# Optimization experiments

Hardware: AMD Instinct MI355X
Metric: run time of the kernel (lower is better)

## Reference

```python
import jax, jax.numpy as jnp
import numpy as np

D = 512      # latent channels (d)
K = 512      # codebook size (k)
PATCH = 8    # encoder conv kernel/stride


def _nearest_embed(z, W):
    """z: (B, D, H, W) latents; W: (D, K) codebook. Returns (quantized (B,D,H,W), argmin (B,H,W))."""
    B, d, H, Wd = z.shape
    zf = z.transpose(0, 2, 3, 1).reshape(-1, d)                      # (N, D)
    # squared L2 distances to each code: ||z||^2 - 2 z.W + ||e||^2
    d2 = (jnp.sum(zf * zf, axis=1, keepdims=True)
          - 2.0 * (zf @ W)
          + jnp.sum(W * W, axis=0))                                   # (N, K)
    idx = jnp.argmin(d2, axis=1)                                      # (N,)
    q = jnp.take(W.T, idx, axis=0)                                    # gather: (N, D)
    q = q.reshape(B, H, Wd, d).transpose(0, 3, 1, 2)
    return q, idx.reshape(B, H, Wd)


def _encode(x, enc_w, enc_b):
    z = jax.lax.conv_general_dilated(x, enc_w, window_strides=(PATCH, PATCH),
                                     padding='VALID',
                                     dimension_numbers=('NCHW', 'OIHW', 'NCHW'))
    return z + enc_b[None, :, None, None]


def _decode(z, dec_w, dec_b):
    y = jax.lax.conv_transpose(z, dec_w, strides=(PATCH, PATCH), padding='VALID',
                               dimension_numbers=('NCHW', 'IOHW', 'NCHW'))
    return y + dec_b[None, :, None, None]


def setup_inputs() -> dict:
    key = jax.random.key(0)
    k1, k2, k3, k4 = jax.random.split(key, 4)
    x = jax.random.normal(k1, (32, 3, 256, 256), dtype=jnp.float32)
    enc_w = jax.random.normal(k2, (D, 3, PATCH, PATCH), dtype=jnp.float32) * 0.02
    enc_b = jnp.zeros((D,), jnp.float32)
    dec_w = jax.random.normal(k3, (D, 3, PATCH, PATCH), dtype=jnp.float32) * 0.02  # IOHW
    dec_b = jnp.zeros((3,), jnp.float32)
    # embedding.weight.normal_(0, 0.02); torch.fmod(weight, 0.04)
    emb_w = jnp.fmod(jax.random.normal(k4, (D, K), dtype=jnp.float32) * 0.02, 0.04)
    return {"x": x, "enc_w": enc_w, "enc_b": enc_b,
            "dec_w": dec_w, "dec_b": dec_b, "emb_w": emb_w}


def reference(x, enc_w, enc_b, dec_w, dec_b, emb_w):
    z_e = _encode(x, enc_w, enc_b)                                    # (32, 512, 32, 32)
    # lookup 1: weight_sg=True (codebook grad stopped) + straight-through estimator
    q1, argmin = _nearest_embed(z_e, jax.lax.stop_gradient(emb_w))
    z_q = z_e + jax.lax.stop_gradient(q1 - z_e)
    # lookup 2: detached encoder output, grads flow to codebook via scatter-add
    emb, _ = _nearest_embed(jax.lax.stop_gradient(z_e), emb_w)
    recon = _decode(z_q, dec_w, dec_b)                                # (32, 3, 256, 256)
    return recon, z_e, emb, argmin
```

## Files before the change

### kernel.cpp

```cpp
#include <hip/hip_runtime.h>
#include <cfloat>

#define PIXB 1024
static const size_t OFF_Z = 6291456;
static const size_t OFF_E = 23068672;
static const size_t OFF_A = 39845888;

typedef __attribute__((address_space(1))) const unsigned int cg_u32;
typedef __attribute__((address_space(3))) unsigned int l_u32;
typedef _Float16 f16x8 __attribute__((ext_vector_type(8)));
typedef _Float16 f16x4 __attribute__((ext_vector_type(4)));
typedef float f32x16 __attribute__((ext_vector_type(16)));

#define SPLIT_SCALE 4096.0f
#define SPLIT_INV   (1.0f / 4096.0f)

#define GL16(srcp, dstp) __builtin_amdgcn_global_load_lds((cg_u32*)(srcp), (l_u32*)(dstp), 16, 0, 0)

__global__ __launch_bounds__(256) void k_prep(const float* __restrict__ W,
                                              const float* __restrict__ dw,
                                              const float* __restrict__ ew,
                                              _Float16* __restrict__ wq,
                                              float* __restrict__ w2,
                                              _Float16* __restrict__ aq,
                                              _Float16* __restrict__ wrow,
                                              _Float16* __restrict__ dwh,
                                              int do_aux) {
  const int t = threadIdx.x;
  const int bx = blockIdx.x;
  __shared__ float T[64][65];
  __shared__ float T2[128][65];
  if (bx < 32) {
    __shared__ float TS[32][260];
    const int cp = bx >> 4, ch = bx & 15;
#pragma unroll
    for (int i = 0; i < 32; ++i)
      TS[i][t] = W[(size_t)(ch * 32 + i) * 512 + cp * 256 + t];
    __syncthreads();
#pragma unroll
    for (int j = 0; j < 4; ++j) {
      const int u = j * 256 + t;
      const int c = u >> 2, slot = u & 3;
      const int se = slot ^ ((c >> 1) & 3);
      f16x8 h, l;
#pragma unroll
      for (int jj = 0; jj < 8; ++jj) {
        const float v = TS[slot * 8 + jj][c];
        const _Float16 hh = (_Float16)v;
        h[jj] = hh;
        l[jj] = (_Float16)((v - (float)hh) * SPLIT_SCALE);
      }
      _Float16* base = wq + cp * 262144 + ch * 16384 + c * 32 + se * 8;
      *(f16x8*)(base) = h;
      *(f16x8*)(base + 8192) = l;
    }
    return;
  }
  if (bx < 34) {
    const int k = (bx - 32) * 256 + t;
    float acc = 0.f;
    for (int d = 0; d < 512; ++d) { const float v = W[(size_t)d * 512 + k]; acc = fmaf(v, v, acc); }
    w2[k] = acc;
    return;
  }
  if (bx < 46) {
    const int ch = bx - 34;
#pragma unroll
    for (int cc = 0; cc < 2; ++cc) {
      const int c = cc * 256 + t;
      const float* src = ew + (size_t)c * 192 + ch * 16;
#pragma unroll
      for (int slot = 0; slot < 2; ++slot) {
        f16x8 h, l;
#pragma unroll
        for (int j = 0; j < 8; ++j) {
          const float v = src[slot * 8 + j];
          const _Float16 hh = (_Float16)v;
          h[j] = hh;
          l[j] = (_Float16)((v - (float)hh) * SPLIT_SCALE);
        }
        const int se = slot ^ ((c >> 2) & 1);
        _Float16* dst = aq + (size_t)ch * 16384 + c * 16 + se * 8;
        *(f16x8*)dst = h;
        *(f16x8*)(dst + 8192) = l;
      }
    }
    return;
  }
  if (!do_aux) return;
  if (bx < 110) {
    const int id = bx - 46;
    const int c0 = (id & 7) * 64, d0 = (id >> 3) * 64;
#pragma unroll
    for (int i = 0; i < 16; ++i) {
      const int dl = i * 4 + (t >> 6);
      T[dl][t & 63] = W[(size_t)(d0 + dl) * 512 + c0 + (t & 63)];
    }
    __syncthreads();
#pragma unroll
    for (int i = 0; i < 16; ++i) {
      const int cl = i * 4 + (t >> 6);
      const int dl = t & 63;
      wrow[(size_t)(c0 + cl) * 512 + d0 + dl] = (_Float16)T[dl][cl];
    }
    return;
  }
  {
    const int id = bx - 110;
    const int m0 = (id % 3) * 64, d0 = (id / 3) * 128;
#pragma unroll
    for (int i = 0; i < 32; ++i) {
      const int idx = i * 256 + t;
      const int dl = idx >> 6, ml = idx & 63;
      T2[dl][ml] = dw[(size_t)(d0 + dl) * 192 + m0 + ml];
    }
    __syncthreads();
#pragma unroll
    for (int i = 0; i < 32; ++i) {
      const int idx = i * 256 + t;
      const int ml = idx >> 7, dl = idx & 127;
      dwh[(size_t)(m0 + ml) * 512 + d0 + dl] = (_Float16)T2[dl][ml];
    }
  }
}

__global__ __launch_bounds__(512) void k_encmfma(const float* __restrict__ x,
                                                 const _Float16* __restrict__ aq,
                                                 const float* __restrict__ eb,
                                                 _Float16* __restrict__ zq2,
                                                 float* __restrict__ out) {
  __shared__ __align__(16) unsigned char CB[131072];
  __shared__ float ebL[512];
  const int t = threadIdx.x;
  ebL[t] = eb[t];
  const int w = t >> 6, lane = t & 63;
  const int wc = w & 3, wp = w >> 2;
  const int n0 = blockIdx.x * 64;
  const int b = n0 >> 10, pixbase = n0 & 1023;
  const int i0 = pixbase >> 5;
  const int row = lane & 31, hi = lane >> 5;

  int ab[4];
#pragma unroll
  for (int ct = 0; ct < 4; ++ct) {
    const int c = wc * 128 + ct * 32 + row;
    ab[ct] = c * 32 + ((hi ^ ((c >> 2) & 1)) << 4);
  }
  const int u = t & 255, srow = u >> 6, vsl = u & 63;
  const int csrc = vsl ^ ((vsl >> 3) & 1);
  const float* xb = x + ((size_t)b * 3 * 256 + (i0 + (srow >> 1)) * 8 + (srow & 1)) * 256 + csrc * 4;
  const int bv0 = (((2 * row) ^ ((row >> 2) & 1)) << 4);
  const int bv1 = (((2 * row + 1) ^ ((row >> 2) & 1)) << 4);
  const int brb = wp * 4096 + (wp * 2 + hi) * 1024;

  f32x16 accA[4], accB[4];
#pragma unroll
  for (int ct = 0; ct < 4; ++ct) { accA[ct] = (f32x16)(0.0f); accB[ct] = (f32x16)(0.0f); }

#define STAGE_A(chv) { const _Float16* as_ = aq + (size_t)(chv) * 16384 + t * 8;            \
    char* ad_ = (char*)CB + ((chv) % 3) * 32768 + t * 16;                                   \
    GL16(as_, ad_); GL16(as_ + 4096, ad_ + 8192);                                           \
    GL16(as_ + 8192, ad_ + 16384); GL16(as_ + 12288, ad_ + 24576); }
#define STAGE_B(chv) GL16(xb + (((chv) >> 2) * 65536 + ((chv) & 3) * 512),                  \
                          (char*)CB + 98304 + (((chv) & 3)) * 8192 + t * 16)
#define ECOMP(chv)                                                                          \
  { const char* abuf = (const char*)CB + ((chv) % 3) * 32768;                               \
    const char* bbuf = (const char*)CB + 98304 + ((chv) & 3) * 8192 + brb;                  \
    const float4 xa = *(const float4*)(bbuf + bv0);                                         \
    const float4 xc = *(const float4*)(bbuf + bv1);                                         \
    const float xs[8] = {xa.x, xa.y, xa.z, xa.w, xc.x, xc.y, xc.z, xc.w};                   \
    f16x8 Bh, Bl;                                                                           \
    _Pragma("unroll") for (int q = 0; q < 8; ++q) {                                         \
      const _Float16 hh = (_Float16)xs[q];                                                  \
      Bh[q] = hh; Bl[q] = (_Float16)((xs[q] - (float)hh) * SPLIT_SCALE); }                  \
    __builtin_amdgcn_s_setprio(1);                                                          \
    _Pragma("unroll") for (int ct_ = 0; ct_ < 4; ++ct_) {                                   \
      const f16x8 Ah = *(const f16x8*)(abuf + ab[ct_]);                                     \
      const f16x8 Al = *(const f16x8*)(abuf + 16384 + ab[ct_]);                             \
      accA[ct_] = __builtin_amdgcn_mfma_f32_32x32x16_f16(Ah, Bh, accA[ct_], 0, 0, 0);       \
      accB[ct_] = __builtin_amdgcn_mfma_f32_32x32x16_f16(Ah, Bl, accB[ct_], 0, 0, 0);       \
      accB[ct_] = __builtin_amdgcn_mfma_f32_32x32x16_f16(Al, Bh, accB[ct_], 0, 0, 0); }     \
    __builtin_amdgcn_s_setprio(0); }
#define EPHASE(chv, waitlit)                                                                \
  { asm volatile("s_waitcnt vmcnt(" #waitlit ")" ::: "memory");                             \
    __builtin_amdgcn_sched_barrier(0);                                                      \
    __builtin_amdgcn_s_barrier();                                                           \
    ECOMP(chv);                                                                             \
    __builtin_amdgcn_s_barrier(); }

  STAGE_A(0); STAGE_B(0);
  STAGE_A(1); STAGE_B(1);
  STAGE_B(2);
#pragma unroll 1
  for (int ch = 0; ch < 9; ++ch) {
    STAGE_A(ch + 2);
    STAGE_B(ch + 3);
    EPHASE(ch, 11);
  }
  STAGE_A(11);
  EPHASE(9, 10);
  EPHASE(10, 5);
  EPHASE(11, 0);
#undef STAGE_A
#undef STAGE_B
#undef ECOMP
#undef EPHASE

  __syncthreads();
  _Float16* ZB = (_Float16*)CB;
  const int pl = wp * 32 + row;
#pragma unroll
  for (int ct = 0; ct < 4; ++ct) {
    float zv[16];
#pragma unroll
    for (int r = 0; r < 16; ++r) {
      const int c = wc * 128 + ct * 32 + (r & 3) + ((r >> 2) << 3) + (hi << 2);
      zv[r] = fmaf(accB[ct][r], SPLIT_INV, accA[ct][r]) + ebL[c];
      out[OFF_Z + ((size_t)(b * 512 + c)) * 1024 + pixbase + pl] = zv[r];
    }
#pragma unroll
    for (int rq = 0; rq < 4; ++rq) {
      f16x4 vh, vl;
#pragma unroll
      for (int q = 0; q < 4; ++q) {
        const float f = zv[rq * 4 + q];
        const _Float16 hh = (_Float16)f;
        vh[q] = hh;
        vl[q] = (_Float16)((f - (float)hh) * SPLIT_SCALE);
      }
      const int c4 = wc * 128 + ct * 32 + (rq << 3) + (hi << 2);
      const int off = pl * 1024 + ((c4 * 2) ^ ((pl & 7) << 4));
      *(f16x4*)((char*)ZB + off) = vh;
      *(f16x4*)((char*)ZB + 65536 + off) = vl;
    }
  }
  __syncthreads();
#pragma unroll
  for (int spl = 0; spl < 2; ++spl)
#pragma unroll
    for (int gg = 0; gg < 8; ++gg) {
      const int g = w * 8 + gg;
      const f16x8 vv = *(const f16x8*)((char*)ZB + spl * 65536 + lane * 1024 + ((g * 16) ^ ((lane & 7) << 4)));
      *(f16x8*)(zq2 + ((size_t)(spl * 64 + g) * 32768 + b * 1024 + pixbase + lane) * 8) = vv;
    }
}

__global__ __launch_bounds__(512) void k_dist(const _Float16* __restrict__ wq,
                                              const _Float16* __restrict__ zq,
                                              const float* __restrict__ w2ws,
                                              float* __restrict__ out) {
  __shared__ __align__(16) unsigned char CB[131072];
  __shared__ float WV[512];
  __shared__ int   WI[512];
  const int t = threadIdx.x;
  const int w = t >> 6, lane = t & 63;
  const int wc = w & 3, wp = w >> 2;
  const int n0 = blockIdx.x * 64;
  const int b = n0 >> 10, pixbase = n0 & 1023;
  const int row = lane & 31, hi = lane >> 5;
  const int kl16 = hi << 4;
  const int pl = wp * 32 + row;

  int abase[2][2];
#pragma unroll
  for (int ct = 0; ct < 2; ++ct) {
    const int cl = wc * 64 + ct * 32 + row;
    const int sw = ((cl >> 1) & 3) << 4;
#pragma unroll
    for (int ks = 0; ks < 2; ++ks)
      abase[ct][ks] = cl * 64 + (((ks << 5) | kl16) ^ sw);
  }
  const _Float16* zsrc0 = zq + ((size_t)((t >> 8) * 64 + ((t >> 6) & 3)) * 32768 +
                                b * 1024 + pixbase + (t & 63)) * 8;

#define STAGE_W(cpv, chv)                                                        \
  { const _Float16* ws_ = wq + (cpv) * 262144 + (chv) * 16384 + t * 8;           \
    char* wd_ = (char*)CB + ((chv) % 3) * 32768 + t * 16;                        \
    GL16(ws_, wd_); GL16(ws_ + 4096, wd_ + 8192);                                \
    GL16(ws_ + 8192, wd_ + 16384); GL16(ws_ + 12288, wd_ + 24576); }
#define STAGE_Z(chv)                                                             \
  GL16(zsrc0 + (size_t)(chv) * 1048576,                                          \
       (char*)CB + 98304 + ((chv) & 3) * 8192 + t * 16)
#define COMPUTE(chv)                                                             \
  { const char* wb_ = (const char*)CB + ((chv) % 3) * 32768;                     \
    const char* zb_ = (const char*)CB + 98304 + ((chv) & 3) * 8192;              \
    const f16x8 Bh0 = *(const f16x8*)(zb_ + hi * 1024 + pl * 16);                \
    const f16x8 Bh1 = *(const f16x8*)(zb_ + (2 + hi) * 1024 + pl * 16);          \
    const f16x8 Bl0 = *(const f16x8*)(zb_ + 4096 + hi * 1024 + pl * 16);         \
    const f16x8 Bl1 = *(const f16x8*)(zb_ + 4096 + (2 + hi) * 1024 + pl * 16);   \
    __builtin_amdgcn_s_setprio(1);                                               \
    _Pragma("unroll")                                                            \
    for (int ct_ = 0; ct_ < 2; ++ct_) {                                          \
      const f16x8 Ah0 = *(const f16x8*)(wb_ + abase[ct_][0]);                    \
      const f16x8 Al0 = *(const f16x8*)(wb_ + 16384 + abase[ct_][0]);            \
      const f16x8 Ah1 = *(const f16x8*)(wb_ + abase[ct_][1]);                    \
      const f16x8 Al1 = *(const f16x8*)(wb_ + 16384 + abase[ct_][1]);            \
      accA[ct_] = __builtin_amdgcn_mfma_f32_32x32x16_f16(Ah0, Bh0, accA[ct_], 0, 0, 0); \
      accB[ct_] = __builtin_amdgcn_mfma_f32_32x32x16_f16(Ah0, Bl0, accB[ct_], 0, 0, 0); \
      accB[ct_] = __builtin_amdgcn_mfma_f32_32x32x16_f16(Al0, Bh0, accB[ct_], 0, 0, 0); \
      accA[ct_] = __builtin_amdgcn_mfma_f32_32x32x16_f16(Ah1, Bh1, accA[ct_], 0, 0, 0); \
      accB[ct_] = __builtin_amdgcn_mfma_f32_32x32x16_f16(Ah1, Bl1, accB[ct_], 0, 0, 0); \
      accB[ct_] = __builtin_amdgcn_mfma_f32_32x32x16_f16(Al1, Bh1, accB[ct_], 0, 0, 0); \
    }                                                                            \
    __builtin_amdgcn_s_setprio(0); }
#define PHASE(chv, waitlit)                                                      \
  { asm volatile("s_waitcnt vmcnt(" #waitlit ")" ::: "memory");                  \
    __builtin_amdgcn_sched_barrier(0);                                           \
    __builtin_amdgcn_s_barrier();                                                \
    COMPUTE(chv);                                                                \
    __builtin_amdgcn_s_barrier(); }

  float bv = FLT_MAX; int bi = 0x7fffffff;

#pragma unroll 1
  for (int cp = 0; cp < 2; ++cp) {
    f32x16 accA[2], accB[2];
#pragma unroll
    for (int ct = 0; ct < 2; ++ct) { accA[ct] = (f32x16)(0.0f); accB[ct] = (f32x16)(0.0f); }
    STAGE_W(cp, 0); STAGE_Z(0);
    STAGE_W(cp, 1); STAGE_Z(1);
    STAGE_Z(2);
#pragma unroll 1
    for (int ch = 0; ch < 13; ++ch) {
      STAGE_W(cp, ch + 2);
      STAGE_Z(ch + 3);
      PHASE(ch, 11);
    }
    STAGE_W(cp, 15);
    PHASE(13, 10);
    PHASE(14, 5);
    PHASE(15, 0);

#pragma unroll
    for (int ct = 0; ct < 2; ++ct) {
#pragma unroll
      for (int r = 0; r < 16; ++r) {
        const int code = cp * 256 + wc * 64 + ct * 32 +
                         ((r & 3) + ((r >> 2) << 3) + (hi << 2));
        const float zw = fmaf(accB[ct][r], SPLIT_INV, accA[ct][r]);
        const float d2 = fmaf(-2.f, zw, w2ws[code]);
        if (d2 < bv || (d2 == bv && code < bi)) { bv = d2; bi = code; }
      }
    }
  }
#undef STAGE_W
#undef STAGE_Z
#undef COMPUTE
#undef PHASE

  WV[w * 64 + lane] = bv;
  WI[w * 64 + lane] = bi;
  __syncthreads();
  if (t < 64) {
    const int pw = t >> 5;
    float fbv = FLT_MAX; int fbi = 0x7fffffff;
#pragma unroll
    for (int wcc = 0; wcc < 4; ++wcc)
#pragma unroll
      for (int hh = 0; hh < 2; ++hh) {
        const int li = (pw * 4 + wcc) * 64 + (t & 31) + hh * 32;
        const float v = WV[li];
        const int ii = WI[li];
        if (v < fbv || (v == fbv && ii < fbi)) { fbv = v; fbi = ii; }
      }
    out[OFF_A + n0 + t] = (float)fbi;
  }
}

__global__ __launch_bounds__(256) void k_gather(const float* __restrict__ Wc,
                                                float* __restrict__ out) {
  const int n0 = blockIdx.x * 32;
  const int b = n0 >> 10, pixbase = n0 & 1023;
  const int t = threadIdx.x;
  const int pix = t & 31;
  const int kidx = (int)out[OFF_A + n0 + pix];
  for (int d = t >> 5; d < 512; d += 8)
    out[OFF_E + ((size_t)(b * 512 + d)) * 1024 + pixbase + pix] = Wc[(size_t)d * 512 + kidx];
}

__global__ __launch_bounds__(512) void k_decmfma(const _Float16* __restrict__ wrow,
                                                 const _Float16* __restrict__ dwh,
                                                 const float* __restrict__ db,
                                                 float* __restrict__ out) {
  __shared__ __align__(16) _Float16 QB[2][4096];
  __shared__ int KIDX[128];
  const int t = threadIdx.x;
  const int w = t >> 6, lane = t & 63;
  const int pt = w & 3, mg = w >> 2;
  const int blk = blockIdx.x;
  const int b = blk >> 3;
  const int pixbase = (blk & 7) * 128;
  if (t < 128) KIDX[t] = (int)out[OFF_A + b * 1024 + pixbase + t];
  __syncthreads();
  const int pixS = t >> 2, slotS = t & 3;
  const _Float16* qsrc = wrow + (size_t)KIDX[pixS] * 512 + slotS * 8;
  const int ldsW = pixS * 32 + (slotS ^ ((pixS >> 1) & 3)) * 8;

  const _Float16* abp[3];
#pragma unroll
  for (int mt = 0; mt < 3; ++mt)
    abp[mt] = dwh + (size_t)((mg * 3 + mt) * 32 + (lane & 31)) * 512 + ((lane >> 5) << 3);

  const int brow = pt * 32 + (lane & 31);
  const int bsw = (brow >> 1) & 3;
  int boff[2];
#pragma unroll
  for (int ks = 0; ks < 2; ++ks)
    boff[ks] = brow * 32 + (((ks * 2 + (lane >> 5)) ^ bsw)) * 8;

  f32x16 acc[3];
#pragma unroll
  for (int mt = 0; mt < 3; ++mt) acc[mt] = (f32x16)(0.0f);
  f16x8 A[2][3][2];
  f16x8 qd[2];

  qd[0] = *(const f16x8*)(qsrc);
#pragma unroll
  for (int mt = 0; mt < 3; ++mt)
#pragma unroll
    for (int ks = 0; ks < 2; ++ks)
      A[0][mt][ks] = *(const f16x8*)(abp[mt] + ks * 16);
  *(f16x8*)&QB[0][ldsW] = qd[0];
  qd[1] = *(const f16x8*)(qsrc + 32);
  __syncthreads();

#pragma unroll
  for (int ch = 0; ch < 16; ++ch) {
    const int par = ch & 1;
    if (ch < 15) {
      *(f16x8*)&QB[par ^ 1][ldsW] = qd[(ch + 1) & 1];
#pragma unroll
      for (int mt = 0; mt < 3; ++mt)
#pragma unroll
        for (int ks = 0; ks < 2; ++ks)
          A[par ^ 1][mt][ks] = *(const f16x8*)(abp[mt] + (ch + 1) * 32 + ks * 16);
    }
    if (ch < 14) qd[ch & 1] = *(const f16x8*)(qsrc + (ch + 2) * 32);
    const f16x8 B0 = *(const f16x8*)&QB[par][boff[0]];
    const f16x8 B1 = *(const f16x8*)&QB[par][boff[1]];
#pragma unroll
    for (int mt = 0; mt < 3; ++mt) {
      acc[mt] = __builtin_amdgcn_mfma_f32_32x32x16_f16(A[par][mt][0], B0, acc[mt], 0, 0, 0);
      acc[mt] = __builtin_amdgcn_mfma_f32_32x32x16_f16(A[par][mt][1], B1, acc[mt], 0, 0, 0);
    }
    __syncthreads();
  }

  const float b0 = db[0], b1 = db[1], b2 = db[2];
  const int pix = pixbase + pt * 32 + (lane & 31);
  const int i = pix >> 5, j = pix & 31;
#pragma unroll
  for (int mt = 0; mt < 3; ++mt) {
    const int m0 = (mg * 3 + mt) * 32;
#pragma unroll
    for (int r = 0; r < 16; ++r) {
      const int m = m0 + (r & 3) + ((r >> 2) << 3) + ((lane >> 5) << 2);
      const int c = m >> 6, ki = (m >> 3) & 7, kj = m & 7;
      const float bias = (c == 0) ? b0 : ((c == 1) ? b1 : b2);
      out[(((size_t)b * 3 + c) * 256 + i * 8 + 7 - ki) * 256 + j * 8 + 7 - kj] = acc[mt][r] + bias;
    }
  }
}

__global__ __launch_bounds__(256) void k_decode(const float* __restrict__ dw,
                                                const float* __restrict__ db,
                                                float* out) {
  __shared__ __align__(16) float Qs[32][132];
  __shared__ __align__(16) float Ws3[32][68];
  const int n0 = blockIdx.x * 128;
  const int b = n0 / PIXB, pixbase = n0 % PIXB;
  const int mt = blockIdx.y;
  const int t = threadIdx.x;
  const int pg = t & 31, ck = t >> 5;
  float acc[4][8];
#pragma unroll
  for (int p = 0; p < 4; ++p)
#pragma unroll
    for (int k = 0; k < 8; ++k) acc[p][k] = 0.f;
  for (int dc = 0; dc < 16; ++dc) {
#pragma unroll
    for (int ii = 0; ii < 4; ++ii) {
      const int id = t + ii * 256;
      const int dd = id >> 5, p4 = id & 31;
      *reinterpret_cast<float4*>(&Qs[dd][p4 * 4]) =
        *reinterpret_cast<const float4*>(&out[OFF_E + ((size_t)b * 512 + dc * 32 + dd) * 1024 + pixbase + p4 * 4]);
    }
#pragma unroll
    for (int ii = 0; ii < 2; ++ii) {
      const int id = t + ii * 256;
      const int dd = id >> 4, m4 = id & 15;
      *reinterpret_cast<float4*>(&Ws3[dd][m4 * 4]) =
        *reinterpret_cast<const float4*>(&dw[(size_t)(dc * 32 + dd) * 192 + mt * 64 + m4 * 4]);
    }
    __syncthreads();
#pragma unroll
    for (int dd = 0; dd < 32; ++dd) {
      const float4 qv = *reinterpret_cast<const float4*>(&Qs[dd][pg * 4]);
      const float4 wa = *reinterpret_cast<const float4*>(&Ws3[dd][ck * 8]);
      const float4 wb = *reinterpret_cast<const float4*>(&Ws3[dd][ck * 8 + 4]);
      const float q[4] = {qv.x, qv.y, qv.z, qv.w};
      const float wv[8] = {wa.x, wa.y, wa.z, wa.w, wb.x, wb.y, wb.z, wb.w};
#pragma unroll
      for (int p = 0; p < 4; ++p)
#pragma unroll
        for (int k = 0; k < 8; ++k) acc[p][k] = fmaf(q[p], wv[k], acc[p][k]);
    }
    __syncthreads();
  }
  const int ckg = mt * 8 + ck;
  const int c = ckg >> 3, ki = ckg & 7;
  const float bias = db[c];
#pragma unroll
  for (int p = 0; p < 4; ++p) {
    const int pix = pixbase + pg * 4 + p;
    const int i = pix >> 5, j = pix & 31;
    const size_t base = (((size_t)b * 3 + c) * 256 + i * 8 + 7 - ki) * 256 + j * 8;
#pragma unroll
    for (int kj = 0; kj < 8; ++kj) out[base + 7 - kj] = acc[p][kj] + bias;
  }
}

extern "C" void kernel_launch(void* const* d_in, const int* in_sizes, int n_in,
                              void* d_out, int out_size, void* d_ws, size_t ws_size,
                              hipStream_t stream) {
  const float* x     = (const float*)d_in[0];
  const float* enc_w = (const float*)d_in[1];
  const float* enc_b = (const float*)d_in[2];
  const float* dec_w = (const float*)d_in[3];
  const float* dec_b = (const float*)d_in[4];
  const float* emb_w = (const float*)d_in[5];
  float* out = (float*)d_out;
  float* w2 = (float*)d_ws;
  _Float16* wrow = (_Float16*)((char*)d_ws + 2048);
  _Float16* dwh  = (_Float16*)((char*)d_ws + 2048 + 524288);
  const int do_aux = (ws_size >= (size_t)(2048 + 524288 + 196608)) ? 1 : 0;
  _Float16* wq  = (_Float16*)d_out;
  _Float16* aq  = (_Float16*)((char*)d_out + 2097152);
  _Float16* zq2 = (_Float16*)((char*)d_out + 92274688);

  k_prep<<<122, 256, 0, stream>>>(emb_w, dec_w, enc_w, wq, w2, aq, wrow, dwh, do_aux);
  k_encmfma<<<512, 512, 0, stream>>>(x, aq, enc_b, zq2, out);
  k_dist<<<512, 512, 0, stream>>>(wq, zq2, w2, out);
  k_gather<<<1024, 256, 0, stream>>>(emb_w, out);
  if (do_aux)
    k_decmfma<<<256, 512, 0, stream>>>(wrow, dwh, dec_b, out);
  else
    k_decode<<<dim3(256, 3), 256, 0, stream>>>(dec_w, dec_b, out);
}
```

Before: 208.4 us.

## Read fp32 z_e directly in distance kernel and fuse codebook gather

The encoder no longer writes a separate split-fp16 (hi/lo) copy of z_e to scratch. The distance kernel now stages the fp32 z_e output tile into LDS and does the hi/lo fp16 split on the fly before the MFMAs. The separate gather kernel is folded into the tail of the distance kernel, which keeps argmin indices in shared memory. This removes a scratch write and read pass plus one launch, in exchange for extra conversion ALU work inside the MFMA loop and a possibly bank-conflicted LDS access pattern for the fp32 reads.

```diff
diff --git a/kernel.cpp b/kernel.cpp
--- a/kernel.cpp
+++ b/kernel.cpp
@@ -9,7 +9,6 @@
 typedef __attribute__((address_space(1))) const unsigned int cg_u32;
 typedef __attribute__((address_space(3))) unsigned int l_u32;
 typedef _Float16 f16x8 __attribute__((ext_vector_type(8)));
-typedef _Float16 f16x4 __attribute__((ext_vector_type(4)));
 typedef float f32x16 __attribute__((ext_vector_type(16)));
 
 #define SPLIT_SCALE 4096.0f
@@ -127,7 +126,6 @@
 __global__ __launch_bounds__(512) void k_encmfma(const float* __restrict__ x,
                                                  const _Float16* __restrict__ aq,
                                                  const float* __restrict__ eb,
-                                                 _Float16* __restrict__ zq2,
                                                  float* __restrict__ out) {
   __shared__ __align__(16) unsigned char CB[131072];
   __shared__ float ebL[512];
@@ -206,59 +204,32 @@
 #undef ECOMP
 #undef EPHASE
 
-  __syncthreads();
-  _Float16* ZB = (_Float16*)CB;
   const int pl = wp * 32 + row;
 #pragma unroll
   for (int ct = 0; ct < 4; ++ct) {
-    float zv[16];
 #pragma unroll
     for (int r = 0; r < 16; ++r) {
       const int c = wc * 128 + ct * 32 + (r & 3) + ((r >> 2) << 3) + (hi << 2);
-      zv[r] = fmaf(accB[ct][r], SPLIT_INV, accA[ct][r]) + ebL[c];
-      out[OFF_Z + ((size_t)(b * 512 + c)) * 1024 + pixbase + pl] = zv[r];
-    }
-#pragma unroll
-    for (int rq = 0; rq < 4; ++rq) {
-      f16x4 vh, vl;
-#pragma unroll
-      for (int q = 0; q < 4; ++q) {
-        const float f = zv[rq * 4 + q];
-        const _Float16 hh = (_Float16)f;
-        vh[q] = hh;
-        vl[q] = (_Float16)((f - (float)hh) * SPLIT_SCALE);
-      }
-      const int c4 = wc * 128 + ct * 32 + (rq << 3) + (hi << 2);
-      const int off = pl * 1024 + ((c4 * 2) ^ ((pl & 7) << 4));
-      *(f16x4*)((char*)ZB + off) = vh;
-      *(f16x4*)((char*)ZB + 65536 + off) = vl;
-    }
-  }
-  __syncthreads();
-#pragma unroll
-  for (int spl = 0; spl < 2; ++spl)
-#pragma unroll
-    for (int gg = 0; gg < 8; ++gg) {
-      const int g = w * 8 + gg;
-      const f16x8 vv = *(const f16x8*)((char*)ZB + spl * 65536 + lane * 1024 + ((g * 16) ^ ((lane & 7) << 4)));
-      *(f16x8*)(zq2 + ((size_t)(spl * 64 + g) * 32768 + b * 1024 + pixbase + lane) * 8) = vv;
-    }
+      out[OFF_Z + ((size_t)(b * 512 + c)) * 1024 + pixbase + pl] =
+          fmaf(accB[ct][r], SPLIT_INV, accA[ct][r]) + ebL[c];
+    }
+  }
 }
 
 __global__ __launch_bounds__(512) void k_dist(const _Float16* __restrict__ wq,
-                                              const _Float16* __restrict__ zq,
+                                              const float* __restrict__ Wc,
                                               const float* __restrict__ w2ws,
                                               float* __restrict__ out) {
   __shared__ __align__(16) unsigned char CB[131072];
   __shared__ float WV[512];
   __shared__ int   WI[512];
+  __shared__ int   IDX[64];
   const int t = threadIdx.x;
   const int w = t >> 6, lane = t & 63;
   const int wc = w & 3, wp = w >> 2;
   const int n0 = blockIdx.x * 64;
   const int b = n0 >> 10, pixbase = n0 & 1023;
   const int row = lane & 31, hi = lane >> 5;
-  const int kl16 = hi << 4;
   const int pl = wp * 32 + row;
 
   int abase[2][2];
@@ -268,10 +239,9 @@
     const int sw = ((cl >> 1) & 3) << 4;
 #pragma unroll
     for (int ks = 0; ks < 2; ++ks)
-      abase[ct][ks] = cl * 64 + (((ks << 5) | kl16) ^ sw);
-  }
-  const _Float16* zsrc0 = zq + ((size_t)((t >> 8) * 64 + ((t >> 6) & 3)) * 32768 +
-                                b * 1024 + pixbase + (t & 63)) * 8;
+      abase[ct][ks] = cl * 64 + (((ks << 5) | (hi << 4)) ^ sw);
+  }
+  const float* zsrc = out + OFF_Z + ((size_t)(b * 512 + (t >> 4))) * 1024 + pixbase + (t & 15) * 4;
 
 #define STAGE_W(cpv, chv)                                                        \
   { const _Float16* ws_ = wq + (cpv) * 262144 + (chv) * 16384 + t * 8;           \
@@ -279,15 +249,19 @@
     GL16(ws_, wd_); GL16(ws_ + 4096, wd_ + 8192);                                \
     GL16(ws_ + 8192, wd_ + 16384); GL16(ws_ + 12288, wd_ + 24576); }
 #define STAGE_Z(chv)                                                             \
-  GL16(zsrc0 + (size_t)(chv) * 1048576,                                          \
+  GL16(zsrc + (size_t)(chv) * 32768,                                             \
        (char*)CB + 98304 + ((chv) & 3) * 8192 + t * 16)
 #define COMPUTE(chv)                                                             \
   { const char* wb_ = (const char*)CB + ((chv) % 3) * 32768;                     \
     const char* zb_ = (const char*)CB + 98304 + ((chv) & 3) * 8192;              \
-    const f16x8 Bh0 = *(const f16x8*)(zb_ + hi * 1024 + pl * 16);                \
-    const f16x8 Bh1 = *(const f16x8*)(zb_ + (2 + hi) * 1024 + pl * 16);          \
-    const f16x8 Bl0 = *(const f16x8*)(zb_ + 4096 + hi * 1024 + pl * 16);         \
-    const f16x8 Bl1 = *(const f16x8*)(zb_ + 4096 + (2 + hi) * 1024 + pl * 16);   \
+    f16x8 Bh0, Bl0, Bh1, Bl1;                                                    \
+    _Pragma("unroll") for (int q = 0; q < 8; ++q) {                              \
+      const float f0 = *(const float*)(zb_ + (hi * 8 + q) * 256 + pl * 4);       \
+      const _Float16 h0 = (_Float16)f0;                                          \
+      Bh0[q] = h0; Bl0[q] = (_Float16)((f0 - (float)h0) * SPLIT_SCALE);          \
+      const float f1 = *(const float*)(zb_ + (16 + hi * 8 + q) * 256 + pl * 4);  \
+      const _Float16 h1 = (_Float16)f1;                                          \
+      Bh1[q] = h1; Bl1[q] = (_Float16)((f1 - (float)h1) * SPLIT_SCALE); }        \
     __builtin_amdgcn_s_setprio(1);                                               \
     _Pragma("unroll")                                                            \
     for (int ct_ = 0; ct_ < 2; ++ct_) {                                          \
@@ -364,17 +338,13 @@
         if (v < fbv || (v == fbv && ii < fbi)) { fbv = v; fbi = ii; }
       }
     out[OFF_A + n0 + t] = (float)fbi;
-  }
-}
-
-__global__ __launch_bounds__(256) void k_gather(const float* __restrict__ Wc,
-                                                float* __restrict__ out) {
-  const int n0 = blockIdx.x * 32;
-  const int b = n0 >> 10, pixbase = n0 & 1023;
-  const int t = threadIdx.x;
-  const int pix = t & 31;
-  const int kidx = (int)out[OFF_A + n0 + pix];
-  for (int d = t >> 5; d < 512; d += 8)
+    IDX[t] = fbi;
+  }
+  __syncthreads();
+
+  const int pix = t & 63;
+  const int kidx = IDX[pix];
+  for (int d = t >> 6; d < 512; d += 8)
     out[OFF_E + ((size_t)(b * 512 + d)) * 1024 + pixbase + pix] = Wc[(size_t)d * 512 + kidx];
 }
 
@@ -536,12 +506,10 @@
   const int do_aux = (ws_size >= (size_t)(2048 + 524288 + 196608)) ? 1 : 0;
   _Float16* wq  = (_Float16*)d_out;
   _Float16* aq  = (_Float16*)((char*)d_out + 2097152);
-  _Float16* zq2 = (_Float16*)((char*)d_out + 92274688);
 
   k_prep<<<122, 256, 0, stream>>>(emb_w, dec_w, enc_w, wq, w2, aq, wrow, dwh, do_aux);
-  k_encmfma<<<512, 512, 0, stream>>>(x, aq, enc_b, zq2, out);
-  k_dist<<<512, 512, 0, stream>>>(wq, zq2, w2, out);
-  k_gather<<<1024, 256, 0, stream>>>(emb_w, out);
+  k_encmfma<<<512, 512, 0, stream>>>(x, aq, enc_b, out);
+  k_dist<<<512, 512, 0, stream>>>(wq, emb_w, w2, out);
   if (do_aux)
     k_decmfma<<<256, 512, 0, stream>>>(wrow, dwh, dec_b, out);
   else
```

Measured after the change: 192.8 us. -7.5%, faster.
